# Performance work log

Measured on AMD Instinct MI355X. Metric: run time of the kernel, lower is better.

Reference implementation:

```python
import jax, jax.numpy as jnp
import numpy as np

N, E, L = 20000, 640000, 2
D_IN, D_H, D_FF = 1546, 128, 512  # in_channels, heads*out_channels, ff_dim
EPS = 1e-5
SLOPE = 0.01  # LeakyReLU default negative slope


def layer_norm(x, g, b):
    m = x.mean(-1, keepdims=True)
    v = ((x - m) ** 2).mean(-1, keepdims=True)
    return (x - m) / jnp.sqrt(v + EPS) * g + b


def setup_inputs() -> dict:
    key = jax.random.key(0)
    ks = iter(jax.random.split(key, 40))
    f32 = jnp.float32
    def w(shape, scale=0.05):
        return jax.random.normal(next(ks), shape, dtype=f32) * scale
    inp = {
        "x": jax.random.normal(next(ks), (N, D_IN), dtype=f32),
        "edge_index": jax.random.randint(next(ks), (2, E), 0, N, dtype=jnp.int64),
        "edge_attr": jax.random.normal(next(ks), (E, D_H), dtype=f32),
        # per-layer TransformerConv params, stacked over L layers
        "Wq": w((L, D_IN, D_H)), "bq": jnp.zeros((L, D_H), f32),
        "Wk": w((L, D_IN, D_H)), "bk": jnp.zeros((L, D_H), f32),
        "Wv": w((L, D_IN, D_H)), "bv": jnp.zeros((L, D_H), f32),
        "Wr": w((L, D_IN, D_H)), "br": jnp.zeros((L, D_H), f32),
        "Whi": w((L, D_IN, D_H)), "Whj": w((L, D_IN, D_H)),
        # per-layer FFMLP params
        "W1": w((L, D_H, D_FF)), "b1": jnp.zeros((L, D_FF), f32),
        "W2": w((L, D_FF, D_H)), "b2": jnp.zeros((L, D_H), f32),
        "g1": jnp.ones((L, D_H), f32), "be1": jnp.zeros((L, D_H), f32),
        "g2": jnp.ones((L, D_H), f32), "be2": jnp.zeros((L, D_H), f32),
        # shared linear 128->1546 and final linear2 1546->128
        "linW": w((D_H, D_IN)), "linb": jnp.zeros((D_IN,), f32),
        "lin2W": w((D_IN, D_H)), "lin2b": jnp.zeros((D_H,), f32),
    }
    return inp


def reference(x, edge_index, edge_attr, Wq, bq, Wk, bk, Wv, bv, Wr, br,
              Whi, Whj, W1, b1, W2, b2, g1, be1, g2, be2,
              linW, linb, lin2W, lin2b):
    src = edge_index[0]  # j (source)
    dst = edge_index[1]  # i (target)
    for l in range(L):
        q = x @ Wq[l] + bq[l]          # [N, D_H]
        k = x @ Wk[l] + bk[l]
        v = x @ Wv[l] + bv[l]
        hi = x @ Whi[l]
        hj = x @ Whj[l]
        # edge gate (uses raw edge_attr, matching original forward)
        gate = jax.nn.sigmoid(edge_attr + hi[src] + hj[dst])      # [E, D_H]
        # per-edge scalar attention, softmax over ALL edges (dim=0, as in source)
        attn = jnp.sum(q[dst] * k[src], axis=-1, keepdims=True)   # [E, 1]
        attn = jax.nn.softmax(attn, axis=0)
        msg = attn * v[src] * gate                                 # [E, D_H]
        aggr = jax.ops.segment_sum(msg, dst, num_segments=N)       # [N, D_H]
        h = aggr + x @ Wr[l] + br[l]   # root weight, concat=False -> no out_proj
        # FFMLP (pre-norm residual on normalized input)
        ss = layer_norm(h, g1[l], be1[l])
        ss2 = jax.nn.relu(ss @ W1[l] + b1[l]) @ W2[l] + b2[l]
        h = layer_norm(ss + ss2, g2[l], be2[l])
        x = h @ linW + linb            # shared 128 -> 1546
    x = jax.nn.leaky_relu(x @ lin2W + lin2b, SLOPE)
    return x
```

## Files before the change

kernel.cpp:

```cpp
#include <hip/hip_runtime.h>
#include <cfloat>
#include <cmath>

#define NN 20000
#define EE 640000
#define DIN 1546
#define KIN 1568
#define DH 128
#define DFF 512
#define NL 2
#define NPROJ 768
#define ALB 2048

typedef unsigned short ushort_t;
typedef __attribute__((ext_vector_type(8))) short short8;
typedef __attribute__((ext_vector_type(8))) unsigned short ushort8;
typedef __attribute__((ext_vector_type(4))) float floatx4;

__device__ inline ushort_t f2bf(float f) {
  unsigned u = __float_as_uint(f);
  unsigned r = (u + 0x7FFF + ((u >> 16) & 1)) >> 16;
  return (ushort_t)r;
}
__device__ inline float bflo(unsigned u) { return __uint_as_float(u << 16); }
__device__ inline float bfhi(unsigned u) { return __uint_as_float(u & 0xFFFF0000u); }

__global__ __launch_bounds__(256) void gemm_bf16(
    const ushort_t* __restrict__ A, int lda,
    const ushort_t* __restrict__ Bt, int ldb,
    const float* __restrict__ bias, void* __restrict__ Cv, int ldc,
    int M, int Nstore, int K, int act, int out_bf16)
{
  __shared__ ushort_t As[4 * 1032];
  __shared__ ushort_t Bs[4 * 1032];
  const int tid = threadIdx.x;
  const int wave = tid >> 6, lane = tid & 63;
  const int bm = blockIdx.x * 128, bn = blockIdx.y * 128;
  const int wm = (wave >> 1) * 64, wn = (wave & 1) * 64;
  const int frow = lane & 15, kq = lane >> 4;

  floatx4 acc[4][4];
  #pragma unroll
  for (int i = 0; i < 4; ++i)
    #pragma unroll
    for (int j = 0; j < 4; ++j) acc[i][j] = (floatx4){0.f, 0.f, 0.f, 0.f};

  const int srow = tid >> 2, skc = tid & 3;
  const int ar0 = min(bm + srow, M - 1);
  const int ar1 = min(bm + srow + 64, M - 1);
  const ushort_t* Ap0 = A + (size_t)ar0 * lda + skc * 8;
  const ushort_t* Ap1 = A + (size_t)ar1 * lda + skc * 8;
  const ushort_t* Bp0 = Bt + (size_t)(bn + srow) * ldb + skc * 8;
  const ushort_t* Bp1 = Bt + (size_t)(bn + srow + 64) * ldb + skc * 8;
  ushort_t* Aw0 = As + skc * 1032 + srow * 8;
  ushort_t* Aw1 = As + skc * 1032 + (srow + 64) * 8;
  ushort_t* Bw0 = Bs + skc * 1032 + srow * 8;
  ushort_t* Bw1 = Bs + skc * 1032 + (srow + 64) * 8;

  for (int k0 = 0; k0 < K; k0 += 32) {
    ushort8 a0 = *(const ushort8*)Ap0; Ap0 += 32;
    ushort8 a1 = *(const ushort8*)Ap1; Ap1 += 32;
    ushort8 b0 = *(const ushort8*)Bp0; Bp0 += 32;
    ushort8 b1 = *(const ushort8*)Bp1; Bp1 += 32;
    __syncthreads();
    *(ushort8*)Aw0 = a0; *(ushort8*)Aw1 = a1;
    *(ushort8*)Bw0 = b0; *(ushort8*)Bw1 = b1;
    __syncthreads();
    short8 af[4], bfv[4];
    #pragma unroll
    for (int i = 0; i < 4; ++i)
      af[i] = *(const short8*)(As + kq * 1032 + (wm + i * 16 + frow) * 8);
    #pragma unroll
    for (int j = 0; j < 4; ++j)
      bfv[j] = *(const short8*)(Bs + kq * 1032 + (wn + j * 16 + frow) * 8);
    #pragma unroll
    for (int i = 0; i < 4; ++i)
      #pragma unroll
      for (int j = 0; j < 4; ++j)
        acc[i][j] = __builtin_amdgcn_mfma_f32_16x16x32_bf16(af[i], bfv[j], acc[i][j], 0, 0, 0);
  }

  const int rq = (lane >> 4) * 4;
  #pragma unroll
  for (int j = 0; j < 4; ++j) {
    int col = bn + wn + j * 16 + frow;
    if (col >= Nstore) continue;
    float bb = bias ? bias[col] : 0.f;
    #pragma unroll
    for (int i = 0; i < 4; ++i) {
      #pragma unroll
      for (int r = 0; r < 4; ++r) {
        int row = bm + wm + i * 16 + rq + r;
        if (row >= M) continue;
        float v = acc[i][j][r] + bb;
        if (act == 1) v = fmaxf(v, 0.f);
        else if (act == 2) v = v > 0.f ? v : 0.01f * v;
        if (out_bf16) ((ushort_t*)Cv)[(size_t)row * ldc + col] = f2bf(v);
        else          ((float*)Cv)[(size_t)row * ldc + col] = v;
      }
    }
  }
}

__global__ __launch_bounds__(256) void convert_x_kernel(
    const float* __restrict__ x, ushort_t* __restrict__ xb)
{
  const unsigned CPR = KIN / 8;
  unsigned gid = blockIdx.x * 256 + threadIdx.x;
  if (gid >= (unsigned)NN * CPR) return;
  unsigned row = gid / CPR;
  unsigned c8 = (gid - row * CPR) * 8;
  const float* xr = x + (size_t)row * DIN;
  ushort8 o;
  #pragma unroll
  for (int j = 0; j < 8; ++j)
    o[j] = (c8 + j < DIN) ? f2bf(xr[c8 + j]) : (ushort_t)0;
  *(ushort8*)(xb + (size_t)row * KIN + c8) = o;
}

__global__ __launch_bounds__(256) void pack6t_kernel(
    const float* __restrict__ Wq, const float* __restrict__ Wk,
    const float* __restrict__ Wv, const float* __restrict__ Wr,
    const float* __restrict__ Whi, const float* __restrict__ Whj,
    ushort_t* __restrict__ Wt6)
{
  __shared__ float tile[32][33];
  const int k0 = blockIdx.x * 32;
  const int n0 = blockIdx.y * 32;
  const float* Ws[6] = {Wq, Wk, Wv, Wr, Whi, Whj};
  const float* W = Ws[n0 >> 7];
  const int c0 = n0 & 127;
  const int tc = threadIdx.x & 31, tr = threadIdx.x >> 5;
  #pragma unroll
  for (int r = tr; r < 32; r += 8) {
    int k = k0 + r;
    tile[r][tc] = (k < DIN) ? W[(size_t)k * DH + c0 + tc] : 0.f;
  }
  __syncthreads();
  #pragma unroll
  for (int n = tr; n < 32; n += 8)
    Wt6[(size_t)(n0 + n) * KIN + k0 + tc] = f2bf(tile[tc][n]);
}

__global__ void pack_bt_kernel(const float* __restrict__ src, ushort_t* __restrict__ dst,
                               int Nsrc, int Ksrc, int Kp) {
  int k = blockIdx.x * 256 + threadIdx.x;
  int n = blockIdx.y;
  if (k >= Kp) return;
  float v = (n < Nsrc && k < Ksrc) ? src[(size_t)k * Nsrc + n] : 0.f;
  dst[(size_t)n * Kp + k] = f2bf(v);
}

__global__ void pack_bias_kernel(const float* __restrict__ bq, const float* __restrict__ bk,
                                 const float* __restrict__ bv, const float* __restrict__ br,
                                 float* __restrict__ out) {
  int n = blockIdx.x * 256 + threadIdx.x;
  if (n >= NPROJ) return;
  int which = n >> 7, c = n & 127;
  float v = 0.f;
  if (which == 0) v = bq[c]; else if (which == 1) v = bk[c];
  else if (which == 2) v = bv[c]; else if (which == 3) v = br[c];
  out[n] = v;
}

__global__ __launch_bounds__(256) void combine6_kernel(
    const float* __restrict__ Wq, const float* __restrict__ Wk,
    const float* __restrict__ Wv, const float* __restrict__ Wr,
    const float* __restrict__ Whi, const float* __restrict__ Whj,
    const float* __restrict__ bq, const float* __restrict__ bk,
    const float* __restrict__ bv, const float* __restrict__ br,
    const float* __restrict__ linW, const float* __restrict__ linb,
    ushort_t* __restrict__ Pc, float* __restrict__ bc)
{
  const int j = threadIdx.x >> 7;
  const int k = threadIdx.x & 127;
  const int n = blockIdx.x * 2 + j;
  const int which = n >> 7, col = n & 127;
  const float* Ws[6] = {Wq, Wk, Wv, Wr, Whi, Whj};
  const float* W = Ws[which];
  __shared__ float wcol[2][DIN];
  for (int d = k; d < DIN; d += 128)
    wcol[j][d] = W[(size_t)d * DH + col];
  __syncthreads();
  const float* lr = linW + (size_t)k * DIN;
  float acc = 0.f;
  #pragma unroll 4
  for (int d = 0; d < DIN; d += 2) {
    float2 lv = *(const float2*)(lr + d);
    acc = fmaf(wcol[j][d], lv.x, acc);
    acc = fmaf(wcol[j][d + 1], lv.y, acc);
  }
  Pc[(size_t)n * DH + k] = f2bf(acc);
  float bs = 0.f;
  for (int d = k; d < DIN; d += 128) bs += linb[d] * wcol[j][d];
  #pragma unroll
  for (int m = 32; m >= 1; m >>= 1) bs += __shfl_xor(bs, m);
  __shared__ float red[4];
  if ((threadIdx.x & 63) == 0) red[threadIdx.x >> 6] = bs;
  __syncthreads();
  if (k == 0) {
    float b0 = 0.f;
    if (which == 0) b0 = bq[col]; else if (which == 1) b0 = bk[col];
    else if (which == 2) b0 = bv[col]; else if (which == 3) b0 = br[col];
    bc[n] = b0 + red[j * 2] + red[j * 2 + 1];
  }
}

__global__ __launch_bounds__(256) void combine_fin_kernel(
    const float* __restrict__ lin2W, const float* __restrict__ lin2b,
    const float* __restrict__ linW, const float* __restrict__ linb,
    ushort_t* __restrict__ Pf, float* __restrict__ bf_out)
{
  const int j = threadIdx.x >> 7;
  const int k = threadIdx.x & 127;
  const int c = blockIdx.x * 2 + j;
  __shared__ float wcol[2][DIN];
  for (int d = k; d < DIN; d += 128)
    wcol[j][d] = lin2W[(size_t)d * DH + c];
  __syncthreads();
  const float* lr = linW + (size_t)k * DIN;
  float acc = 0.f;
  #pragma unroll 4
  for (int d = 0; d < DIN; d += 2) {
    float2 lv = *(const float2*)(lr + d);
    acc = fmaf(wcol[j][d], lv.x, acc);
    acc = fmaf(wcol[j][d + 1], lv.y, acc);
  }
  Pf[(size_t)c * DH + k] = f2bf(acc);
  float bs = 0.f;
  for (int d = k; d < DIN; d += 128) bs += linb[d] * wcol[j][d];
  #pragma unroll
  for (int m = 32; m >= 1; m >>= 1) bs += __shfl_xor(bs, m);
  __shared__ float red[4];
  if ((threadIdx.x & 63) == 0) red[threadIdx.x >> 6] = bs;
  __syncthreads();
  if (k == 0) bf_out[c] = lin2b[c] + red[j * 2] + red[j * 2 + 1];
}

__global__ void hist_kernel(const int* __restrict__ ei, int* __restrict__ counts) {
  int e = blockIdx.x * 256 + threadIdx.x;
  if (e < EE) atomicAdd(&counts[ei[EE + e]], 1);
}

__global__ __launch_bounds__(1024) void scan_kernel(const int* __restrict__ counts,
                                                    int* __restrict__ offsets,
                                                    int* __restrict__ cursor) {
  __shared__ int sums[1024];
  const int t = threadIdx.x;
  const int PER = 20;
  int base = t * PER;
  int loc[PER]; int s = 0;
  #pragma unroll
  for (int i = 0; i < PER; ++i) {
    int idx = base + i;
    int c = (idx < NN) ? counts[idx] : 0;
    loc[i] = s; s += c;
  }
  sums[t] = s;
  __syncthreads();
  for (int d = 1; d < 1024; d <<= 1) {
    int v = (t >= d) ? sums[t - d] : 0;
    __syncthreads();
    sums[t] += v;
    __syncthreads();
  }
  int pre = (t > 0) ? sums[t - 1] : 0;
  #pragma unroll
  for (int i = 0; i < PER; ++i) {
    int idx = base + i;
    if (idx < NN) { offsets[idx] = pre + loc[i]; cursor[idx] = pre + loc[i]; }
  }
  if (t == 0) offsets[NN] = sums[1023];
}

__global__ void scatter_kernel(const int* __restrict__ ei, int* __restrict__ cursor,
                               int* __restrict__ csr) {
  int e = blockIdx.x * 256 + threadIdx.x;
  if (e < EE) {
    int p = atomicAdd(&cursor[ei[EE + e]], 1);
    csr[p] = e;
  }
}

__device__ inline void atomicMaxF(float* addr, float val) {
  if (val >= 0.f) atomicMax((int*)addr, __float_as_int(val));
  else            atomicMin((unsigned int*)addr, __float_as_uint(val));
}

__global__ void init_scalars(float* scal) {
  if (threadIdx.x < NL) { scal[threadIdx.x * 2] = -INFINITY; scal[threadIdx.x * 2 + 1] = 0.f; }
}

__global__ __launch_bounds__(256) void attn_logits(
    const int* __restrict__ ei, const ushort_t* __restrict__ qkv,
    float* __restrict__ s_e, float* __restrict__ scal)
{
  const int tid = threadIdx.x;
  const int l = tid & 31;
  const int ngroups = ALB * 8;
  const int g = blockIdx.x * 8 + (tid >> 5);
  float mx = -FLT_MAX;
  for (int e = g; e < EE; e += 2 * ngroups) {
    const int e2 = e + ngroups;
    const bool has2 = (e2 < EE);
    int src1 = ei[e], dst1 = ei[EE + e];
    int src2 = has2 ? ei[e2] : src1;
    int dst2 = has2 ? ei[EE + e2] : dst1;
    uint2 qu1 = *(const uint2*)(qkv + (size_t)dst1 * NPROJ + l * 4);
    uint2 ku1 = *(const uint2*)(qkv + (size_t)src1 * NPROJ + DH + l * 4);
    uint2 qu2 = *(const uint2*)(qkv + (size_t)dst2 * NPROJ + l * 4);
    uint2 ku2 = *(const uint2*)(qkv + (size_t)src2 * NPROJ + DH + l * 4);
    float d1 = bflo(qu1.x) * bflo(ku1.x) + bfhi(qu1.x) * bfhi(ku1.x)
             + bflo(qu1.y) * bflo(ku1.y) + bfhi(qu1.y) * bfhi(ku1.y);
    float d2 = bflo(qu2.x) * bflo(ku2.x) + bfhi(qu2.x) * bfhi(ku2.x)
             + bflo(qu2.y) * bflo(ku2.y) + bfhi(qu2.y) * bfhi(ku2.y);
    #pragma unroll
    for (int m = 16; m >= 1; m >>= 1) {
      d1 += __shfl_xor(d1, m);
      d2 += __shfl_xor(d2, m);
    }
    if (l == 0) {
      s_e[e] = d1;
      if (has2) s_e[e2] = d2;
    }
    mx = fmaxf(mx, has2 ? fmaxf(d1, d2) : d1);
  }
  mx = fmaxf(mx, __shfl_xor(mx, 32));
  __shared__ float red[4];
  if ((tid & 63) == 0) red[tid >> 6] = mx;
  __syncthreads();
  if (tid == 0)
    atomicMaxF(scal, fmaxf(fmaxf(red[0], red[1]), fmaxf(red[2], red[3])));
}

__global__ __launch_bounds__(256) void exp_sum(
    float* __restrict__ s_e, const float* __restrict__ scal, float* __restrict__ Z)
{
  const int e = blockIdx.x * 256 + threadIdx.x;
  const float mx = scal[0];
  float v = __expf(s_e[e] - mx);
  s_e[e] = v;
  float t = v;
  #pragma unroll
  for (int m = 32; m >= 1; m >>= 1) t += __shfl_xor(t, m);
  __shared__ float red[4];
  if ((threadIdx.x & 63) == 0) red[threadIdx.x >> 6] = t;
  __syncthreads();
  if (threadIdx.x == 0) atomicAdd(Z, red[0] + red[1] + red[2] + red[3]);
}

__global__ __launch_bounds__(256) void aggregate_ln_kernel(
    const int* __restrict__ ei, const int* __restrict__ offsets,
    const int* __restrict__ csr, const float* __restrict__ s_e,
    const float* __restrict__ scal, const ushort_t* __restrict__ qkv,
    const float* __restrict__ ea,
    const float* __restrict__ g, const float* __restrict__ b,
    float* __restrict__ ss, ushort_t* __restrict__ ssbf)
{
  const int node = blockIdx.x * 4 + (threadIdx.x >> 6);
  const int lane = threadIdx.x & 63;
  if (node >= NN) return;
  const int off = offsets[node];
  const int deg = offsets[node + 1] - off;
  const float invZ = 1.f / scal[1];
  const ushort_t* bd = qkv + (size_t)node * NPROJ;
  unsigned hjp = *(const unsigned*)(bd + 640 + lane * 2);
  unsigned rp  = *(const unsigned*)(bd + 384 + lane * 2);
  const float hj0 = bflo(hjp), hj1 = bfhi(hjp);
  float a0 = bflo(rp), a1 = bfhi(rp);
  for (int b0 = 0; b0 < deg; b0 += 64) {
    int t = b0 + lane;
    int eL = (t < deg) ? csr[off + t] : 0;
    int sL = (t < deg) ? ei[eL] : 0;
    float pL = (t < deg) ? s_e[eL] * invZ : 0.f;
    int cnt = min(64, deg - b0);
    for (int u = 0; u < cnt; ++u) {
      int e = __shfl(eL, u);
      int src = __shfl(sL, u);
      float p = __shfl(pL, u);
      const ushort_t* bs = qkv + (size_t)src * NPROJ;
      unsigned vv = *(const unsigned*)(bs + 256 + lane * 2);
      unsigned hv = *(const unsigned*)(bs + 512 + lane * 2);
      float2 eav = *(const float2*)(ea + (size_t)e * DH + lane * 2);
      float g0 = 1.f / (1.f + __expf(-(eav.x + bflo(hv) + hj0)));
      float g1 = 1.f / (1.f + __expf(-(eav.y + bfhi(hv) + hj1)));
      a0 = fmaf(p * bflo(vv), g0, a0);
      a1 = fmaf(p * bfhi(vv), g1, a1);
    }
  }
  float s = a0 + a1;
  #pragma unroll
  for (int m = 32; m >= 1; m >>= 1) s += __shfl_xor(s, m);
  float mean = s * (1.f / 128.f);
  float dx = a0 - mean, dy = a1 - mean;
  float v = dx * dx + dy * dy;
  #pragma unroll
  for (int m = 32; m >= 1; m >>= 1) v += __shfl_xor(v, m);
  float rstd = rsqrtf(v * (1.f / 128.f) + 1e-5f);
  float2 gg = *(const float2*)(g + lane * 2);
  float2 bb = *(const float2*)(b + lane * 2);
  float o0 = dx * rstd * gg.x + bb.x;
  float o1 = dy * rstd * gg.y + bb.y;
  *(float2*)(ss + (size_t)node * DH + lane * 2) = make_float2(o0, o1);
  ushort_t* pp = ssbf + (size_t)node * DH + lane * 2;
  pp[0] = f2bf(o0); pp[1] = f2bf(o1);
}

__global__ __launch_bounds__(256) void ln_kernel(
    const float* __restrict__ X, const float* __restrict__ X2,
    const float* __restrict__ g, const float* __restrict__ b,
    float* __restrict__ Yf, ushort_t* __restrict__ Yb)
{
  int row = blockIdx.x * 4 + (threadIdx.x >> 6);
  int lane = threadIdx.x & 63;
  if (row >= NN) return;
  float2 x = *(const float2*)(X + (size_t)row * DH + lane * 2);
  if (X2) {
    float2 y = *(const float2*)(X2 + (size_t)row * DH + lane * 2);
    x.x += y.x; x.y += y.y;
  }
  float s = x.x + x.y;
  #pragma unroll
  for (int m = 32; m >= 1; m >>= 1) s += __shfl_xor(s, m);
  float mean = s * (1.f / 128.f);
  float dx = x.x - mean, dy = x.y - mean;
  float v = dx * dx + dy * dy;
  #pragma unroll
  for (int m = 32; m >= 1; m >>= 1) v += __shfl_xor(v, m);
  float rstd = rsqrtf(v * (1.f / 128.f) + 1e-5f);
  float2 gg = *(const float2*)(g + lane * 2);
  float2 bb = *(const float2*)(b + lane * 2);
  float o0 = dx * rstd * gg.x + bb.x;
  float o1 = dy * rstd * gg.y + bb.y;
  if (Yf) *(float2*)(Yf + (size_t)row * DH + lane * 2) = make_float2(o0, o1);
  if (Yb) {
    ushort_t* p = Yb + (size_t)row * DH + lane * 2;
    p[0] = f2bf(o0); p[1] = f2bf(o1);
  }
}

extern "C" void kernel_launch(void* const* d_in, const int* in_sizes, int n_in,
                              void* d_out, int out_size, void* d_ws, size_t ws_size,
                              hipStream_t stream)
{
  const float* x_in  = (const float*)d_in[0];
  const int*   ei    = (const int*)d_in[1];
  const float* ea    = (const float*)d_in[2];
  const float* Wq    = (const float*)d_in[3];
  const float* bq    = (const float*)d_in[4];
  const float* Wk    = (const float*)d_in[5];
  const float* bk    = (const float*)d_in[6];
  const float* Wv    = (const float*)d_in[7];
  const float* bv    = (const float*)d_in[8];
  const float* Wr    = (const float*)d_in[9];
  const float* br    = (const float*)d_in[10];
  const float* Whi   = (const float*)d_in[11];
  const float* Whj   = (const float*)d_in[12];
  const float* W1    = (const float*)d_in[13];
  const float* b1    = (const float*)d_in[14];
  const float* W2    = (const float*)d_in[15];
  const float* b2    = (const float*)d_in[16];
  const float* g1    = (const float*)d_in[17];
  const float* be1   = (const float*)d_in[18];
  const float* g2    = (const float*)d_in[19];
  const float* be2   = (const float*)d_in[20];
  const float* linW  = (const float*)d_in[21];
  const float* linb  = (const float*)d_in[22];
  const float* lin2W = (const float*)d_in[23];
  const float* lin2b = (const float*)d_in[24];
  float* out = (float*)d_out;

  char* p = (char*)d_ws;
  auto alloc = [&](size_t bytes) -> void* {
    void* r = (void*)p; p += (bytes + 63) & ~((size_t)63); return r;
  };
  ushort_t* x_bf   = (ushort_t*)alloc((size_t)NN * KIN * 2);
  ushort_t* qkvp   = (ushort_t*)alloc((size_t)NN * NPROJ * 2);
  ushort_t* Wt6    = (ushort_t*)alloc((size_t)NPROJ * KIN * 2);
  ushort_t* W1t    = (ushort_t*)alloc((size_t)DFF * DH * 2);
  ushort_t* W2t    = (ushort_t*)alloc((size_t)DH * DFF * 2);
  ushort_t* Wc6    = (ushort_t*)alloc((size_t)NPROJ * DH * 2);
  ushort_t* Wcf    = (ushort_t*)alloc((size_t)DH * DH * 2);
  float*    bias768= (float*)alloc(NPROJ * 4);
  float*    bc768  = (float*)alloc(NPROJ * 4);
  float*    bcf    = (float*)alloc(DH * 4);
  float*    s_e    = (float*)alloc((size_t)EE * 4);
  float*    scal   = (float*)alloc(64);
  int*      counts = (int*)alloc((size_t)NN * 4);
  int*      offsets= (int*)alloc((size_t)(NN + 1) * 4);
  int*      cursor = (int*)alloc((size_t)NN * 4);
  int*      csr    = (int*)alloc((size_t)EE * 4);
  float*    ss     = (float*)alloc((size_t)NN * DH * 4);
  ushort_t* ssbf   = (ushort_t*)alloc((size_t)NN * DH * 2);
  ushort_t* ff1bf  = (ushort_t*)alloc((size_t)NN * DFF * 2);
  float*    ss2    = (float*)alloc((size_t)NN * DH * 4);
  ushort_t* h2bf   = (ushort_t*)alloc((size_t)NN * DH * 2);

  const dim3 blk(256);
  const int MB = (NN + 127) / 128;

  convert_x_kernel<<<dim3((NN * (KIN / 8) + 255) / 256), blk, 0, stream>>>(x_in, x_bf);
  hipMemsetAsync(counts, 0, (size_t)NN * 4, stream);
  hist_kernel<<<dim3(EE / 256), blk, 0, stream>>>(ei, counts);
  scan_kernel<<<dim3(1), dim3(1024), 0, stream>>>(counts, offsets, cursor);
  scatter_kernel<<<dim3(EE / 256), blk, 0, stream>>>(ei, cursor, csr);

  const size_t wo1 = (size_t)DIN * DH;
  combine6_kernel<<<dim3(NPROJ / 2), blk, 0, stream>>>(
      Wq + wo1, Wk + wo1, Wv + wo1, Wr + wo1, Whi + wo1, Whj + wo1,
      bq + DH, bk + DH, bv + DH, br + DH, linW, linb, Wc6, bc768);
  combine_fin_kernel<<<dim3(DH / 2), blk, 0, stream>>>(
      lin2W, lin2b, linW, linb, Wcf, bcf);
  init_scalars<<<1, 64, 0, stream>>>(scal);

  for (int l = 0; l < NL; ++l) {
    pack_bt_kernel<<<dim3(1, DFF), blk, 0, stream>>>(W1 + (size_t)l * DH * DFF, W1t, DFF, DH, DH);
    pack_bt_kernel<<<dim3(2, DH), blk, 0, stream>>>(W2 + (size_t)l * DFF * DH, W2t, DH, DFF, DFF);

    if (l == 0) {
      pack6t_kernel<<<dim3(KIN / 32, NPROJ / 32), blk, 0, stream>>>(
          Wq, Wk, Wv, Wr, Whi, Whj, Wt6);
      pack_bias_kernel<<<dim3(3), blk, 0, stream>>>(bq, bk, bv, br, bias768);
      gemm_bf16<<<dim3(MB, 6), blk, 0, stream>>>(
          x_bf, KIN, Wt6, KIN, bias768, qkvp, NPROJ, NN, NPROJ, KIN, 0, 1);
    } else {
      gemm_bf16<<<dim3(MB, 6), blk, 0, stream>>>(
          h2bf, DH, Wc6, DH, bc768, qkvp, NPROJ, NN, NPROJ, DH, 0, 1);
    }

    attn_logits<<<dim3(ALB), blk, 0, stream>>>(ei, qkvp, s_e, scal + l * 2);
    exp_sum<<<dim3(EE / 256), blk, 0, stream>>>(s_e, scal + l * 2, scal + l * 2 + 1);
    aggregate_ln_kernel<<<dim3(NN / 4), blk, 0, stream>>>(
        ei, offsets, csr, s_e, scal + l * 2, qkvp, ea,
        g1 + (size_t)l * DH, be1 + (size_t)l * DH, ss, ssbf);

    gemm_bf16<<<dim3(MB, 4), blk, 0, stream>>>(
        ssbf, DH, W1t, DH, b1 + (size_t)l * DFF, ff1bf, DFF, NN, DFF, DH, 1, 1);
    gemm_bf16<<<dim3(MB, 1), blk, 0, stream>>>(
        ff1bf, DFF, W2t, DFF, b2 + (size_t)l * DH, ss2, DH, NN, DH, DFF, 0, 0);
    ln_kernel<<<dim3(NN / 4), blk, 0, stream>>>(ss, ss2, g2 + (size_t)l * DH, be2 + (size_t)l * DH, nullptr, h2bf);
  }

  gemm_bf16<<<dim3(MB, 1), blk, 0, stream>>>(
      h2bf, DH, Wcf, DH, bcf, out, DH, NN, DH, DH, 2, 0);
}
```

Before: 1.584 ms.

## Compute attention logits in CSR order with online softmax; fuse FF2 GEMM with LayerNorm

Attention logits are now computed per destination node in CSR order, with q loaded once per node. A per-block online max/sum-exp is reduced by a single-block kernel, which replaces the global atomic max pass and the separate exp pass. Aggregation recomputes the exp from the stored CSR-ordered logit and reads source ids directly from a CSR source array. The FF2 GEMM is fused with residual add and LayerNorm through an LDS tile, and the small weight-packing and combine kernels are merged into fewer launches. The aim is fewer launches, fewer global round trips and no atomics, at the cost of more LDS in the fused GEMM and an extra exp per edge during aggregation.

```diff
diff --git a/kernel.cpp b/kernel.cpp
--- a/kernel.cpp
+++ b/kernel.cpp
@@ -10,7 +10,7 @@
 #define DFF 512
 #define NL 2
 #define NPROJ 768
-#define ALB 2048
+#define NB (NN / 4)
 
 typedef unsigned short ushort_t;
 typedef __attribute__((ext_vector_type(8))) short short8;
@@ -102,6 +102,104 @@
   }
 }
 
+__global__ __launch_bounds__(256) void gemm_ff2_ln(
+    const ushort_t* __restrict__ A,
+    const ushort_t* __restrict__ Bt,
+    const float* __restrict__ bias,
+    const float* __restrict__ ss,
+    const float* __restrict__ g, const float* __restrict__ b,
+    ushort_t* __restrict__ Yb, int M)
+{
+  __shared__ ushort_t As[4 * 1032];
+  __shared__ ushort_t Bs[4 * 1032];
+  __shared__ float vrow[128][130];
+  const int tid = threadIdx.x;
+  const int wave = tid >> 6, lane = tid & 63;
+  const int bm = blockIdx.x * 128;
+  const int wm = (wave >> 1) * 64, wn = (wave & 1) * 64;
+  const int frow = lane & 15, kq = lane >> 4;
+
+  floatx4 acc[4][4];
+  #pragma unroll
+  for (int i = 0; i < 4; ++i)
+    #pragma unroll
+    for (int j = 0; j < 4; ++j) acc[i][j] = (floatx4){0.f, 0.f, 0.f, 0.f};
+
+  const int srow = tid >> 2, skc = tid & 3;
+  const ushort_t* Ap0 = A + (size_t)min(bm + srow, M - 1) * DFF + skc * 8;
+  const ushort_t* Ap1 = A + (size_t)min(bm + srow + 64, M - 1) * DFF + skc * 8;
+  const ushort_t* Bp0 = Bt + (size_t)srow * DFF + skc * 8;
+  const ushort_t* Bp1 = Bt + (size_t)(srow + 64) * DFF + skc * 8;
+  ushort_t* Aw0 = As + skc * 1032 + srow * 8;
+  ushort_t* Aw1 = As + skc * 1032 + (srow + 64) * 8;
+  ushort_t* Bw0 = Bs + skc * 1032 + srow * 8;
+  ushort_t* Bw1 = Bs + skc * 1032 + (srow + 64) * 8;
+
+  for (int k0 = 0; k0 < DFF; k0 += 32) {
+    ushort8 a0 = *(const ushort8*)Ap0; Ap0 += 32;
+    ushort8 a1 = *(const ushort8*)Ap1; Ap1 += 32;
+    ushort8 b0 = *(const ushort8*)Bp0; Bp0 += 32;
+    ushort8 b1 = *(const ushort8*)Bp1; Bp1 += 32;
+    __syncthreads();
+    *(ushort8*)Aw0 = a0; *(ushort8*)Aw1 = a1;
+    *(ushort8*)Bw0 = b0; *(ushort8*)Bw1 = b1;
+    __syncthreads();
+    short8 af[4], bfv[4];
+    #pragma unroll
+    for (int i = 0; i < 4; ++i)
+      af[i] = *(const short8*)(As + kq * 1032 + (wm + i * 16 + frow) * 8);
+    #pragma unroll
+    for (int j = 0; j < 4; ++j)
+      bfv[j] = *(const short8*)(Bs + kq * 1032 + (wn + j * 16 + frow) * 8);
+    #pragma unroll
+    for (int i = 0; i < 4; ++i)
+      #pragma unroll
+      for (int j = 0; j < 4; ++j)
+        acc[i][j] = __builtin_amdgcn_mfma_f32_16x16x32_bf16(af[i], bfv[j], acc[i][j], 0, 0, 0);
+  }
+
+  const int rq = (lane >> 4) * 4;
+  #pragma unroll
+  for (int j = 0; j < 4; ++j) {
+    int col = wn + j * 16 + frow;
+    float bb = bias[col];
+    #pragma unroll
+    for (int i = 0; i < 4; ++i) {
+      #pragma unroll
+      for (int r = 0; r < 4; ++r) {
+        int row = wm + i * 16 + rq + r;
+        int grow = bm + row;
+        float v = acc[i][j][r] + bb;
+        if (grow < M) v += ss[(size_t)grow * DH + col];
+        vrow[row][col] = v;
+      }
+    }
+  }
+  __syncthreads();
+
+  float2 gg = *(const float2*)(g + lane * 2);
+  float2 bbv = *(const float2*)(b + lane * 2);
+  for (int rr = 0; rr < 32; ++rr) {
+    int row = wave * 32 + rr;
+    int grow = bm + row;
+    if (grow >= M) break;
+    float x0 = vrow[row][lane * 2], x1 = vrow[row][lane * 2 + 1];
+    float s = x0 + x1;
+    #pragma unroll
+    for (int m = 32; m >= 1; m >>= 1) s += __shfl_xor(s, m);
+    float mean = s * (1.f / 128.f);
+    float dx = x0 - mean, dy = x1 - mean;
+    float v = dx * dx + dy * dy;
+    #pragma unroll
+    for (int m = 32; m >= 1; m >>= 1) v += __shfl_xor(v, m);
+    float rstd = rsqrtf(v * (1.f / 128.f) + 1e-5f);
+    float o0 = dx * rstd * gg.x + bbv.x;
+    float o1 = dy * rstd * gg.y + bbv.y;
+    ushort_t* pp = Yb + (size_t)grow * DH + lane * 2;
+    pp[0] = f2bf(o0); pp[1] = f2bf(o1);
+  }
+}
+
 __global__ __launch_bounds__(256) void convert_x_kernel(
     const float* __restrict__ x, ushort_t* __restrict__ xb)
 {
@@ -142,42 +240,57 @@
     Wt6[(size_t)(n0 + n) * KIN + k0 + tc] = f2bf(tile[tc][n]);
 }
 
-__global__ void pack_bt_kernel(const float* __restrict__ src, ushort_t* __restrict__ dst,
-                               int Nsrc, int Ksrc, int Kp) {
-  int k = blockIdx.x * 256 + threadIdx.x;
-  int n = blockIdx.y;
-  if (k >= Kp) return;
-  float v = (n < Nsrc && k < Ksrc) ? src[(size_t)k * Nsrc + n] : 0.f;
-  dst[(size_t)n * Kp + k] = f2bf(v);
-}
-
-__global__ void pack_bias_kernel(const float* __restrict__ bq, const float* __restrict__ bk,
-                                 const float* __restrict__ bv, const float* __restrict__ br,
-                                 float* __restrict__ out) {
-  int n = blockIdx.x * 256 + threadIdx.x;
-  if (n >= NPROJ) return;
-  int which = n >> 7, c = n & 127;
-  float v = 0.f;
-  if (which == 0) v = bq[c]; else if (which == 1) v = bk[c];
-  else if (which == 2) v = bv[c]; else if (which == 3) v = br[c];
-  out[n] = v;
-}
-
-__global__ __launch_bounds__(256) void combine6_kernel(
+__global__ void pack_small_kernel(
+    const float* __restrict__ W1, const float* __restrict__ W2,
+    const float* __restrict__ bq, const float* __restrict__ bk,
+    const float* __restrict__ bv, const float* __restrict__ br,
+    ushort_t* __restrict__ W1t0, ushort_t* __restrict__ W1t1,
+    ushort_t* __restrict__ W2t0, ushort_t* __restrict__ W2t1,
+    float* __restrict__ bias768)
+{
+  const int y = blockIdx.y;
+  const int tid = threadIdx.x;
+  if (y < 1024) {
+    int l = y >> 9, n = y & 511;
+    const float* src = W1 + (size_t)l * DH * DFF;
+    ushort_t* dst = l ? W1t1 : W1t0;
+    if (tid < DH) dst[(size_t)n * DH + tid] = f2bf(src[(size_t)tid * DFF + n]);
+  } else if (y < 1280) {
+    int l = (y - 1024) >> 7, n = (y - 1024) & 127;
+    const float* src = W2 + (size_t)l * DFF * DH;
+    ushort_t* dst = l ? W2t1 : W2t0;
+    for (int k = tid; k < DFF; k += 256)
+      dst[(size_t)n * DFF + k] = f2bf(src[(size_t)k * DH + n]);
+  } else {
+    int n = (y - 1280) * 256 + tid;
+    if (n < NPROJ) {
+      int which = n >> 7, c = n & 127;
+      float v = 0.f;
+      if (which == 0) v = bq[c]; else if (which == 1) v = bk[c];
+      else if (which == 2) v = bv[c]; else if (which == 3) v = br[c];
+      bias768[n] = v;
+    }
+  }
+}
+
+__global__ __launch_bounds__(256) void combine_all_kernel(
     const float* __restrict__ Wq, const float* __restrict__ Wk,
     const float* __restrict__ Wv, const float* __restrict__ Wr,
     const float* __restrict__ Whi, const float* __restrict__ Whj,
     const float* __restrict__ bq, const float* __restrict__ bk,
     const float* __restrict__ bv, const float* __restrict__ br,
+    const float* __restrict__ lin2W, const float* __restrict__ lin2b,
     const float* __restrict__ linW, const float* __restrict__ linb,
-    ushort_t* __restrict__ Pc, float* __restrict__ bc)
+    ushort_t* __restrict__ Pc, float* __restrict__ bc,
+    ushort_t* __restrict__ Pf, float* __restrict__ bf_out)
 {
   const int j = threadIdx.x >> 7;
   const int k = threadIdx.x & 127;
-  const int n = blockIdx.x * 2 + j;
-  const int which = n >> 7, col = n & 127;
+  const bool six = blockIdx.x < (NPROJ / 2);
+  const int n = six ? blockIdx.x * 2 + j : (blockIdx.x - NPROJ / 2) * 2 + j;
   const float* Ws[6] = {Wq, Wk, Wv, Wr, Whi, Whj};
-  const float* W = Ws[which];
+  const float* W = six ? Ws[n >> 7] : lin2W;
+  const int col = six ? (n & 127) : n;
   __shared__ float wcol[2][DIN];
   for (int d = k; d < DIN; d += 128)
     wcol[j][d] = W[(size_t)d * DH + col];
@@ -190,7 +303,8 @@
     acc = fmaf(wcol[j][d], lv.x, acc);
     acc = fmaf(wcol[j][d + 1], lv.y, acc);
   }
-  Pc[(size_t)n * DH + k] = f2bf(acc);
+  if (six) Pc[(size_t)n * DH + k] = f2bf(acc);
+  else     Pf[(size_t)n * DH + k] = f2bf(acc);
   float bs = 0.f;
   for (int d = k; d < DIN; d += 128) bs += linb[d] * wcol[j][d];
   #pragma unroll
@@ -199,42 +313,17 @@
   if ((threadIdx.x & 63) == 0) red[threadIdx.x >> 6] = bs;
   __syncthreads();
   if (k == 0) {
-    float b0 = 0.f;
-    if (which == 0) b0 = bq[col]; else if (which == 1) b0 = bk[col];
-    else if (which == 2) b0 = bv[col]; else if (which == 3) b0 = br[col];
-    bc[n] = b0 + red[j * 2] + red[j * 2 + 1];
-  }
-}
-
-__global__ __launch_bounds__(256) void combine_fin_kernel(
-    const float* __restrict__ lin2W, const float* __restrict__ lin2b,
-    const float* __restrict__ linW, const float* __restrict__ linb,
-    ushort_t* __restrict__ Pf, float* __restrict__ bf_out)
-{
-  const int j = threadIdx.x >> 7;
-  const int k = threadIdx.x & 127;
-  const int c = blockIdx.x * 2 + j;
-  __shared__ float wcol[2][DIN];
-  for (int d = k; d < DIN; d += 128)
-    wcol[j][d] = lin2W[(size_t)d * DH + c];
-  __syncthreads();
-  const float* lr = linW + (size_t)k * DIN;
-  float acc = 0.f;
-  #pragma unroll 4
-  for (int d = 0; d < DIN; d += 2) {
-    float2 lv = *(const float2*)(lr + d);
-    acc = fmaf(wcol[j][d], lv.x, acc);
-    acc = fmaf(wcol[j][d + 1], lv.y, acc);
-  }
-  Pf[(size_t)c * DH + k] = f2bf(acc);
-  float bs = 0.f;
-  for (int d = k; d < DIN; d += 128) bs += linb[d] * wcol[j][d];
-  #pragma unroll
-  for (int m = 32; m >= 1; m >>= 1) bs += __shfl_xor(bs, m);
-  __shared__ float red[4];
-  if ((threadIdx.x & 63) == 0) red[threadIdx.x >> 6] = bs;
-  __syncthreads();
-  if (k == 0) bf_out[c] = lin2b[c] + red[j * 2] + red[j * 2 + 1];
+    float tot = red[j * 2] + red[j * 2 + 1];
+    if (six) {
+      int which = n >> 7, c = n & 127;
+      float b0 = 0.f;
+      if (which == 0) b0 = bq[c]; else if (which == 1) b0 = bk[c];
+      else if (which == 2) b0 = bv[c]; else if (which == 3) b0 = br[c];
+      bc[n] = b0 + tot;
+    } else {
+      bf_out[n] = lin2b[n] + tot;
+    }
+  }
 }
 
 __global__ void hist_kernel(const int* __restrict__ ei, int* __restrict__ counts) {
@@ -274,84 +363,95 @@
 }
 
 __global__ void scatter_kernel(const int* __restrict__ ei, int* __restrict__ cursor,
-                               int* __restrict__ csr) {
+                               int* __restrict__ csrc, int* __restrict__ cea) {
   int e = blockIdx.x * 256 + threadIdx.x;
   if (e < EE) {
+    int src = ei[e];
     int p = atomicAdd(&cursor[ei[EE + e]], 1);
-    csr[p] = e;
-  }
-}
-
-__device__ inline void atomicMaxF(float* addr, float val) {
-  if (val >= 0.f) atomicMax((int*)addr, __float_as_int(val));
-  else            atomicMin((unsigned int*)addr, __float_as_uint(val));
-}
-
-__global__ void init_scalars(float* scal) {
-  if (threadIdx.x < NL) { scal[threadIdx.x * 2] = -INFINITY; scal[threadIdx.x * 2 + 1] = 0.f; }
-}
-
-__global__ __launch_bounds__(256) void attn_logits(
-    const int* __restrict__ ei, const ushort_t* __restrict__ qkv,
-    float* __restrict__ s_e, float* __restrict__ scal)
-{
-  const int tid = threadIdx.x;
-  const int l = tid & 31;
-  const int ngroups = ALB * 8;
-  const int g = blockIdx.x * 8 + (tid >> 5);
-  float mx = -FLT_MAX;
-  for (int e = g; e < EE; e += 2 * ngroups) {
-    const int e2 = e + ngroups;
-    const bool has2 = (e2 < EE);
-    int src1 = ei[e], dst1 = ei[EE + e];
-    int src2 = has2 ? ei[e2] : src1;
-    int dst2 = has2 ? ei[EE + e2] : dst1;
-    uint2 qu1 = *(const uint2*)(qkv + (size_t)dst1 * NPROJ + l * 4);
-    uint2 ku1 = *(const uint2*)(qkv + (size_t)src1 * NPROJ + DH + l * 4);
-    uint2 qu2 = *(const uint2*)(qkv + (size_t)dst2 * NPROJ + l * 4);
-    uint2 ku2 = *(const uint2*)(qkv + (size_t)src2 * NPROJ + DH + l * 4);
-    float d1 = bflo(qu1.x) * bflo(ku1.x) + bfhi(qu1.x) * bfhi(ku1.x)
-             + bflo(qu1.y) * bflo(ku1.y) + bfhi(qu1.y) * bfhi(ku1.y);
-    float d2 = bflo(qu2.x) * bflo(ku2.x) + bfhi(qu2.x) * bfhi(ku2.x)
-             + bflo(qu2.y) * bflo(ku2.y) + bfhi(qu2.y) * bfhi(ku2.y);
-    #pragma unroll
-    for (int m = 16; m >= 1; m >>= 1) {
-      d1 += __shfl_xor(d1, m);
-      d2 += __shfl_xor(d2, m);
-    }
-    if (l == 0) {
-      s_e[e] = d1;
-      if (has2) s_e[e2] = d2;
-    }
-    mx = fmaxf(mx, has2 ? fmaxf(d1, d2) : d1);
-  }
-  mx = fmaxf(mx, __shfl_xor(mx, 32));
-  __shared__ float red[4];
-  if ((tid & 63) == 0) red[tid >> 6] = mx;
+    csrc[p] = src;
+    cea[p] = e;
+  }
+}
+
+__global__ __launch_bounds__(256) void attn_logits_csr(
+    const int* __restrict__ offsets, const int* __restrict__ csrc,
+    const ushort_t* __restrict__ qkv, float* __restrict__ s_csr,
+    float* __restrict__ mb, float* __restrict__ zb)
+{
+  const int node = blockIdx.x * 4 + (threadIdx.x >> 6);
+  const int lane = threadIdx.x & 63;
+  const int sub = lane & 31, hh = lane >> 5;
+  float m = -FLT_MAX, z = 0.f;
+  if (node < NN) {
+    const int off = offsets[node];
+    const int deg = offsets[node + 1] - off;
+    uint2 qu = *(const uint2*)(qkv + (size_t)node * NPROJ + sub * 4);
+    float q0 = bflo(qu.x), q1 = bfhi(qu.x), q2 = bflo(qu.y), q3 = bfhi(qu.y);
+    for (int t = hh; t < deg; t += 2) {
+      int pos = off + t;
+      int src = csrc[pos];
+      uint2 ku = *(const uint2*)(qkv + (size_t)src * NPROJ + DH + sub * 4);
+      float d = q0 * bflo(ku.x) + q1 * bfhi(ku.x) + q2 * bflo(ku.y) + q3 * bfhi(ku.y);
+      #pragma unroll
+      for (int mm = 16; mm >= 1; mm >>= 1) d += __shfl_xor(d, mm);
+      if (sub == 0) s_csr[pos] = d;
+      if (d <= m) z += __expf(d - m);
+      else { z = z * __expf(m - d) + 1.f; m = d; }
+    }
+  }
+  {
+    float mo = __shfl_xor(m, 32), zo = __shfl_xor(z, 32);
+    float mn = fmaxf(m, mo);
+    z = z * __expf(m - mn) + zo * __expf(mo - mn);
+    m = mn;
+  }
+  __shared__ float ms[4], zs[4];
+  if (lane == 0) { ms[threadIdx.x >> 6] = m; zs[threadIdx.x >> 6] = z; }
   __syncthreads();
-  if (tid == 0)
-    atomicMaxF(scal, fmaxf(fmaxf(red[0], red[1]), fmaxf(red[2], red[3])));
-}
-
-__global__ __launch_bounds__(256) void exp_sum(
-    float* __restrict__ s_e, const float* __restrict__ scal, float* __restrict__ Z)
-{
-  const int e = blockIdx.x * 256 + threadIdx.x;
-  const float mx = scal[0];
-  float v = __expf(s_e[e] - mx);
-  s_e[e] = v;
-  float t = v;
-  #pragma unroll
-  for (int m = 32; m >= 1; m >>= 1) t += __shfl_xor(t, m);
-  __shared__ float red[4];
-  if ((threadIdx.x & 63) == 0) red[threadIdx.x >> 6] = t;
+  if (threadIdx.x == 0) {
+    float M4 = fmaxf(fmaxf(ms[0], ms[1]), fmaxf(ms[2], ms[3]));
+    float Z4 = zs[0] * __expf(ms[0] - M4) + zs[1] * __expf(ms[1] - M4)
+             + zs[2] * __expf(ms[2] - M4) + zs[3] * __expf(ms[3] - M4);
+    mb[blockIdx.x] = M4; zb[blockIdx.x] = Z4;
+  }
+}
+
+__global__ __launch_bounds__(1024) void smreduce_kernel(
+    const float* __restrict__ mb, const float* __restrict__ zb,
+    float* __restrict__ scal)
+{
+  const int t = threadIdx.x;
+  float m = -FLT_MAX, z = 0.f;
+  for (int i = t; i < NB; i += 1024) {
+    float mi = mb[i], zi = zb[i];
+    float mn = fmaxf(m, mi);
+    z = z * __expf(m - mn) + zi * __expf(mi - mn);
+    m = mn;
+  }
+  #pragma unroll
+  for (int s = 32; s >= 1; s >>= 1) {
+    float mo = __shfl_xor(m, s), zo = __shfl_xor(z, s);
+    float mn = fmaxf(m, mo);
+    z = z * __expf(m - mn) + zo * __expf(mo - mn);
+    m = mn;
+  }
+  __shared__ float ms[16], zs[16];
+  if ((t & 63) == 0) { ms[t >> 6] = m; zs[t >> 6] = z; }
   __syncthreads();
-  if (threadIdx.x == 0) atomicAdd(Z, red[0] + red[1] + red[2] + red[3]);
+  if (t == 0) {
+    float M = ms[0], Z = zs[0];
+    for (int i = 1; i < 16; ++i) {
+      float mn = fmaxf(M, ms[i]);
+      Z = Z * __expf(M - mn) + zs[i] * __expf(ms[i] - mn);
+      M = mn;
+    }
+    scal[0] = M; scal[1] = Z;
+  }
 }
 
 __global__ __launch_bounds__(256) void aggregate_ln_kernel(
-    const int* __restrict__ ei, const int* __restrict__ offsets,
-    const int* __restrict__ csr, const float* __restrict__ s_e,
+    const int* __restrict__ offsets, const int* __restrict__ csrc,
+    const int* __restrict__ cea, const float* __restrict__ s_csr,
     const float* __restrict__ scal, const ushort_t* __restrict__ qkv,
     const float* __restrict__ ea,
     const float* __restrict__ g, const float* __restrict__ b,
@@ -362,6 +462,7 @@
   if (node >= NN) return;
   const int off = offsets[node];
   const int deg = offsets[node + 1] - off;
+  const float M = scal[0];
   const float invZ = 1.f / scal[1];
   const ushort_t* bd = qkv + (size_t)node * NPROJ;
   unsigned hjp = *(const unsigned*)(bd + 640 + lane * 2);
@@ -370,9 +471,11 @@
   float a0 = bflo(rp), a1 = bfhi(rp);
   for (int b0 = 0; b0 < deg; b0 += 64) {
     int t = b0 + lane;
-    int eL = (t < deg) ? csr[off + t] : 0;
-    int sL = (t < deg) ? ei[eL] : 0;
-    float pL = (t < deg) ? s_e[eL] * invZ : 0.f;
+    bool valid = t < deg;
+    int pos = off + (valid ? t : 0);
+    int sL = valid ? csrc[pos] : 0;
+    int eL = valid ? cea[pos] : 0;
+    float pL = valid ? __expf(s_csr[pos] - M) * invZ : 0.f;
     int cnt = min(64, deg - b0);
     for (int u = 0; u < cnt; ++u) {
       int e = __shfl(eL, u);
@@ -404,39 +507,6 @@
   *(float2*)(ss + (size_t)node * DH + lane * 2) = make_float2(o0, o1);
   ushort_t* pp = ssbf + (size_t)node * DH + lane * 2;
   pp[0] = f2bf(o0); pp[1] = f2bf(o1);
-}
-
-__global__ __launch_bounds__(256) void ln_kernel(
-    const float* __restrict__ X, const float* __restrict__ X2,
-    const float* __restrict__ g, const float* __restrict__ b,
-    float* __restrict__ Yf, ushort_t* __restrict__ Yb)
-{
-  int row = blockIdx.x * 4 + (threadIdx.x >> 6);
-  int lane = threadIdx.x & 63;
-  if (row >= NN) return;
-  float2 x = *(const float2*)(X + (size_t)row * DH + lane * 2);
-  if (X2) {
-    float2 y = *(const float2*)(X2 + (size_t)row * DH + lane * 2);
-    x.x += y.x; x.y += y.y;
-  }
-  float s = x.x + x.y;
-  #pragma unroll
-  for (int m = 32; m >= 1; m >>= 1) s += __shfl_xor(s, m);
-  float mean = s * (1.f / 128.f);
-  float dx = x.x - mean, dy = x.y - mean;
-  float v = dx * dx + dy * dy;
-  #pragma unroll
-  for (int m = 32; m >= 1; m >>= 1) v += __shfl_xor(v, m);
-  float rstd = rsqrtf(v * (1.f / 128.f) + 1e-5f);
-  float2 gg = *(const float2*)(g + lane * 2);
-  float2 bb = *(const float2*)(b + lane * 2);
-  float o0 = dx * rstd * gg.x + bb.x;
-  float o1 = dy * rstd * gg.y + bb.y;
-  if (Yf) *(float2*)(Yf + (size_t)row * DH + lane * 2) = make_float2(o0, o1);
-  if (Yb) {
-    ushort_t* p = Yb + (size_t)row * DH + lane * 2;
-    p[0] = f2bf(o0); p[1] = f2bf(o1);
-  }
 }
 
 extern "C" void kernel_launch(void* const* d_in, const int* in_sizes, int n_in,
@@ -477,23 +547,27 @@
   ushort_t* x_bf   = (ushort_t*)alloc((size_t)NN * KIN * 2);
   ushort_t* qkvp   = (ushort_t*)alloc((size_t)NN * NPROJ * 2);
   ushort_t* Wt6    = (ushort_t*)alloc((size_t)NPROJ * KIN * 2);
-  ushort_t* W1t    = (ushort_t*)alloc((size_t)DFF * DH * 2);
-  ushort_t* W2t    = (ushort_t*)alloc((size_t)DH * DFF * 2);
+  ushort_t* W1t0   = (ushort_t*)alloc((size_t)DFF * DH * 2);
+  ushort_t* W1t1   = (ushort_t*)alloc((size_t)DFF * DH * 2);
+  ushort_t* W2t0   = (ushort_t*)alloc((size_t)DH * DFF * 2);
+  ushort_t* W2t1   = (ushort_t*)alloc((size_t)DH * DFF * 2);
   ushort_t* Wc6    = (ushort_t*)alloc((size_t)NPROJ * DH * 2);
   ushort_t* Wcf    = (ushort_t*)alloc((size_t)DH * DH * 2);
   float*    bias768= (float*)alloc(NPROJ * 4);
   float*    bc768  = (float*)alloc(NPROJ * 4);
   float*    bcf    = (float*)alloc(DH * 4);
-  float*    s_e    = (float*)alloc((size_t)EE * 4);
+  float*    s_csr  = (float*)alloc((size_t)EE * 4);
   float*    scal   = (float*)alloc(64);
   int*      counts = (int*)alloc((size_t)NN * 4);
   int*      offsets= (int*)alloc((size_t)(NN + 1) * 4);
   int*      cursor = (int*)alloc((size_t)NN * 4);
-  int*      csr    = (int*)alloc((size_t)EE * 4);
+  int*      csrc   = (int*)alloc((size_t)EE * 4);
+  int*      cea    = (int*)alloc((size_t)EE * 4);
+  float*    mb     = (float*)alloc((size_t)NB * 4);
+  float*    zb     = (float*)alloc((size_t)NB * 4);
   float*    ss     = (float*)alloc((size_t)NN * DH * 4);
   ushort_t* ssbf   = (ushort_t*)alloc((size_t)NN * DH * 2);
   ushort_t* ff1bf  = (ushort_t*)alloc((size_t)NN * DFF * 2);
-  float*    ss2    = (float*)alloc((size_t)NN * DH * 4);
   ushort_t* h2bf   = (ushort_t*)alloc((size_t)NN * DH * 2);
 
   const dim3 blk(256);
@@ -503,24 +577,19 @@
   hipMemsetAsync(counts, 0, (size_t)NN * 4, stream);
   hist_kernel<<<dim3(EE / 256), blk, 0, stream>>>(ei, counts);
   scan_kernel<<<dim3(1), dim3(1024), 0, stream>>>(counts, offsets, cursor);
-  scatter_kernel<<<dim3(EE / 256), blk, 0, stream>>>(ei, cursor, csr);
-
+  scatter_kernel<<<dim3(EE / 256), blk, 0, stream>>>(ei, cursor, csrc, cea);
+  pack6t_kernel<<<dim3(KIN / 32, NPROJ / 32), blk, 0, stream>>>(
+      Wq, Wk, Wv, Wr, Whi, Whj, Wt6);
+  pack_small_kernel<<<dim3(1, 1283), blk, 0, stream>>>(
+      W1, W2, bq, bk, bv, br, W1t0, W1t1, W2t0, W2t1, bias768);
   const size_t wo1 = (size_t)DIN * DH;
-  combine6_kernel<<<dim3(NPROJ / 2), blk, 0, stream>>>(
+  combine_all_kernel<<<dim3(NPROJ / 2 + DH / 2), blk, 0, stream>>>(
       Wq + wo1, Wk + wo1, Wv + wo1, Wr + wo1, Whi + wo1, Whj + wo1,
-      bq + DH, bk + DH, bv + DH, br + DH, linW, linb, Wc6, bc768);
-  combine_fin_kernel<<<dim3(DH / 2), blk, 0, stream>>>(
-      lin2W, lin2b, linW, linb, Wcf, bcf);
-  init_scalars<<<1, 64, 0, stream>>>(scal);
+      bq + DH, bk + DH, bv + DH, br + DH,
+      lin2W, lin2b, linW, linb, Wc6, bc768, Wcf, bcf);
 
   for (int l = 0; l < NL; ++l) {
-    pack_bt_kernel<<<dim3(1, DFF), blk, 0, stream>>>(W1 + (size_t)l * DH * DFF, W1t, DFF, DH, DH);
-    pack_bt_kernel<<<dim3(2, DH), blk, 0, stream>>>(W2 + (size_t)l * DFF * DH, W2t, DH, DFF, DFF);
-
     if (l == 0) {
-      pack6t_kernel<<<dim3(KIN / 32, NPROJ / 32), blk, 0, stream>>>(
-          Wq, Wk, Wv, Wr, Whi, Whj, Wt6);
-      pack_bias_kernel<<<dim3(3), blk, 0, stream>>>(bq, bk, bv, br, bias768);
       gemm_bf16<<<dim3(MB, 6), blk, 0, stream>>>(
           x_bf, KIN, Wt6, KIN, bias768, qkvp, NPROJ, NN, NPROJ, KIN, 0, 1);
     } else {
@@ -528,17 +597,17 @@
           h2bf, DH, Wc6, DH, bc768, qkvp, NPROJ, NN, NPROJ, DH, 0, 1);
     }
 
-    attn_logits<<<dim3(ALB), blk, 0, stream>>>(ei, qkvp, s_e, scal + l * 2);
-    exp_sum<<<dim3(EE / 256), blk, 0, stream>>>(s_e, scal + l * 2, scal + l * 2 + 1);
-    aggregate_ln_kernel<<<dim3(NN / 4), blk, 0, stream>>>(
-        ei, offsets, csr, s_e, scal + l * 2, qkvp, ea,
+    attn_logits_csr<<<dim3(NB), blk, 0, stream>>>(offsets, csrc, qkvp, s_csr, mb, zb);
+    smreduce_kernel<<<dim3(1), dim3(1024), 0, stream>>>(mb, zb, scal + l * 2);
+    aggregate_ln_kernel<<<dim3(NB), blk, 0, stream>>>(
+        offsets, csrc, cea, s_csr, scal + l * 2, qkvp, ea,
         g1 + (size_t)l * DH, be1 + (size_t)l * DH, ss, ssbf);
 
     gemm_bf16<<<dim3(MB, 4), blk, 0, stream>>>(
-        ssbf, DH, W1t, DH, b1 + (size_t)l * DFF, ff1bf, DFF, NN, DFF, DH, 1, 1);
-    gemm_bf16<<<dim3(MB, 1), blk, 0, stream>>>(
-        ff1bf, DFF, W2t, DFF, b2 + (size_t)l * DH, ss2, DH, NN, DH, DFF, 0, 0);
-    ln_kernel<<<dim3(NN / 4), blk, 0, stream>>>(ss, ss2, g2 + (size_t)l * DH, be2 + (size_t)l * DH, nullptr, h2bf);
+        ssbf, DH, l ? W1t1 : W1t0, DH, b1 + (size_t)l * DFF, ff1bf, DFF, NN, DFF, DH, 1, 1);
+    gemm_ff2_ln<<<dim3(MB, 1), blk, 0, stream>>>(
+        ff1bf, l ? W2t1 : W2t0, b2 + (size_t)l * DH, ss,
+        g2 + (size_t)l * DH, be2 + (size_t)l * DH, h2bf, NN);
   }
 
   gemm_bf16<<<dim3(MB, 1), blk, 0, stream>>>(
```

Result: faster. 1.436 ms (-9.3%).
